# Performance work log

Hardware: AMD Instinct MI355X
Metric: run time of the kernel (lower is better)

The kernel has to match this reference:

```python
import jax, jax.numpy as jnp
import numpy as np

EPS = 1e-6


def _expand_mask(mask, D, H, W):
    # mask: (B,1,f,f,f) bool -> (B,1,D,H,W) via repeat_interleave on each spatial axis
    m = jnp.repeat(mask, D // mask.shape[2], axis=2)
    m = jnp.repeat(m, H // mask.shape[3], axis=3)
    m = jnp.repeat(m, W // mask.shape[4], axis=4)
    return m


def setup_inputs() -> dict:
    key = jax.random.key(0)
    ks = jax.random.split(key, 10)
    B, C, D, H, W = 2, 192, 32, 32, 32
    K, HID = 7, 4 * C
    x = jax.random.normal(ks[0], (B, C, D, H, W), dtype=jnp.float32)
    mask = jax.random.randint(ks[1], (B, 1, 8, 8, 8), 0, 2) > 0
    dw_w = jax.random.normal(ks[2], (C, 1, K, K, K), dtype=jnp.float32) * (1.0 / np.sqrt(K**3))
    dw_b = jnp.zeros((C,), dtype=jnp.float32)
    ln_w = jnp.ones((C,), dtype=jnp.float32)
    ln_b = jnp.zeros((C,), dtype=jnp.float32)
    w1 = jax.random.normal(ks[3], (C, HID), dtype=jnp.float32) * (1.0 / np.sqrt(C))
    b1 = jnp.zeros((HID,), dtype=jnp.float32)
    w2 = jax.random.normal(ks[4], (HID, C), dtype=jnp.float32) * (1.0 / np.sqrt(HID))
    b2 = jnp.zeros((C,), dtype=jnp.float32)
    gamma = jnp.full((C,), 1e-6, dtype=jnp.float32)
    return {"x": x, "mask": mask, "dw_w": dw_w, "dw_b": dw_b, "ln_w": ln_w,
            "ln_b": ln_b, "w1": w1, "b1": b1, "w2": w2, "b2": b2, "gamma": gamma}


def reference(x, mask, dw_w, dw_b, ln_w, ln_b, w1, b1, w2, b2, gamma):
    B, C, D, H, W = x.shape
    m = _expand_mask(mask, D, H, W)              # (B,1,D,H,W) bool
    mf = m.astype(x.dtype)

    # depthwise 3D conv, SAME padding (padding = kernel//2), groups = C
    y = jax.lax.conv_general_dilated(
        x, dw_w, window_strides=(1, 1, 1), padding='SAME',
        dimension_numbers=('NCDHW', 'OIDHW', 'NCDHW'),
        feature_group_count=C)
    y = y + dw_b[None, :, None, None, None]

    # channels_last: (B,D,H,W,C)
    y = jnp.transpose(y, (0, 2, 3, 4, 1))

    # sparse LayerNorm over channel dim: normalize all tokens, keep only active
    # (equivalent to gather->LN->scatter-into-zeros in the original)
    mu = jnp.mean(y, axis=-1, keepdims=True)
    var = jnp.mean(jnp.square(y - mu), axis=-1, keepdims=True)
    ln = (y - mu) * jax.lax.rsqrt(var + EPS) * ln_w + ln_b
    ln = ln * jnp.transpose(mf, (0, 2, 3, 4, 1))  # zero inactive tokens

    # pointwise MLP
    h = jax.nn.gelu(jnp.einsum('bdhwc,ce->bdhwe', ln, w1) + b1, approximate=False)
    o = jnp.einsum('bdhwe,ec->bdhwc', h, w2) + b2
    o = gamma * o

    # back to channels_first and final sparse mask
    o = jnp.transpose(o, (0, 4, 1, 2, 3)) * mf
    return o
```

## Files before the change

kernel.cpp:

```cpp
#include <hip/hip_runtime.h>
#include <hip/hip_bf16.h>

typedef __attribute__((ext_vector_type(2))) float f2v;
typedef __attribute__((ext_vector_type(4))) float f4v;
typedef __attribute__((ext_vector_type(8))) short bf8v;

#define NPOS 32768
#define CCH  192
#define HID  768

#define WS_Y    ((size_t)0)
#define WS_B1F  ((size_t)25165824)
#define WS_B2F  ((size_t)25460736)
#define WS_WPF  ((size_t)25755648)
#define WS_TOTAL ((size_t)26357760)

__device__ inline unsigned short f2bf(float f){
  unsigned int u = __float_as_uint(f);
  u += 0x7FFFu + ((u >> 16) & 1u);
  return (unsigned short)(u >> 16);
}
__device__ inline float bf2f(unsigned short s){
  return __uint_as_float(((unsigned int)s) << 16);
}
__device__ inline float gelu_f(float x){
  float u = 0.7978845608028654f * x * fmaf(0.044715f, x*x, 1.0f);
  float e = __expf(2.0f*u);
  float th = __fdividef(e - 1.0f, e + 1.0f);
  return 0.5f*x*(1.0f + th);
}

#define DOT2(A, X, W) \
  asm("v_dot2_f32_f16 %0, %1, %2, %0" : "+v"(A) : "v"(X), "s"(W))

__global__ __launch_bounds__(256, 6) void conv_dw_f16_kernel(
    const float* __restrict__ x, const float* __restrict__ dw_b,
    const unsigned int* __restrict__ wpf, unsigned short* __restrict__ yc)
{
  __shared__ unsigned short ring[22*528];

  int bid = blockIdx.x;
  int c = bid % 192;
  int r = bid / 192;
  int xq = r & 1, yq = (r >> 1) & 1, zh = (r >> 2) & 1, b = r >> 3;
  int tx0 = xq*16, ty0 = yq*16, zb = zh*16;

  int tid = threadIdx.x;
  const float* xsrc = x + ((size_t)(b*CCH + c))*NPOS;

  for (int idx = tid; idx < 2904; idx += 256) {
    int sl = idx / 132;
    int rem = idx - sl*132;
    int rr = rem / 6, ci = rem - rr*6;
    int zi = zb - 3 + sl, gy = ty0 - 3 + rr, gx = tx0 - 4 + 4*ci;
    f4v v = {0.f, 0.f, 0.f, 0.f};
    if ((unsigned)zi < 32u && (unsigned)gy < 32u && (unsigned)gx <= 28u)
      v = *(const f4v*)(xsrc + (size_t)zi*1024 + gy*32 + gx);
    union { _Float16 h[4]; uint2 u2; } pk;
    pk.h[0] = (_Float16)v[0]; pk.h[1] = (_Float16)v[1];
    pk.h[2] = (_Float16)v[2]; pk.h[3] = (_Float16)v[3];
    *(uint2*)(ring + sl*528 + rr*24 + ci*4) = pk.u2;
  }
  __syncthreads();

  int p = tid & 15, zl = tid >> 4;
  int px = p & 3, py = p >> 2;
  int y0 = py*4, px4 = px*4;
  const unsigned short* base = ring + zl*528 + y0*24 + px4;

  const unsigned int* wb = wpf + (size_t)c*392;

  float acc[4][4];
  #pragma unroll
  for (int i = 0; i < 4; ++i)
    #pragma unroll
    for (int j = 0; j < 4; ++j) acc[i][j] = 0.f;

  #pragma unroll 1
  for (int s = 0; s < 7; ++s) {
    const unsigned short* sb = base + s*528;
    const unsigned int* wrow = wb + s*56;
    #pragma unroll
    for (int rr = 0; rr < 10; ++rr) {
      const unsigned short* rb = sb + rr*24;
      uint2 q0 = *(const uint2*)(rb);
      uint2 q1 = *(const uint2*)(rb + 4);
      uint2 q2 = *(const uint2*)(rb + 8);
      unsigned int D[6] = {q0.x, q0.y, q1.x, q1.y, q2.x, q2.y};
      #pragma unroll
      for (int dy = 0; dy < 4; ++dy) {
        int ky = rr - dy;
        if (ky < 0 || ky > 6) continue;
        const unsigned int* wk = wrow + ky*8;
        #pragma unroll
        for (int t = 0; t < 4; ++t) {
          DOT2(acc[dy][0], D[t],   wk[t]);
          DOT2(acc[dy][1], D[t+1], wk[4+t]);
          DOT2(acc[dy][2], D[t+1], wk[t]);
          DOT2(acc[dy][3], D[t+2], wk[4+t]);
        }
      }
    }
  }

  float bias = dw_b[c];
  int z = zb + zl;
  int cz = z >> 2, cx = (tx0 >> 2) + px, cy = (ty0 >> 2) + py;
  int cell = cz*64 + cy*8 + cx;
  unsigned short* ybase = yc + (((size_t)(b*512 + cell))*192 + c)*64;
  int tokz = (z & 3)*16;
  #pragma unroll
  for (int dy = 0; dy < 4; ++dy) {
    ushort4 o;
    o.x = f2bf(acc[dy][0] + bias);
    o.y = f2bf(acc[dy][1] + bias);
    o.z = f2bf(acc[dy][2] + bias);
    o.w = f2bf(acc[dy][3] + bias);
    *(ushort4*)(ybase + tokz + dy*4) = o;
  }
}

__global__ __launch_bounds__(256) void conv_dw_f32_kernel(
    const float* __restrict__ x, const float* __restrict__ dw_w,
    const float* __restrict__ dw_b, unsigned short* __restrict__ yc)
{
  __shared__ float ring[22*528];

  int bid = blockIdx.x;
  int c = bid % 192;
  int r = bid / 192;
  int xq = r & 1, yq = (r >> 1) & 1, zh = (r >> 2) & 1, b = r >> 3;
  int tx0 = xq*16, ty0 = yq*16, zb = zh*16;

  int tid = threadIdx.x;
  const float* xsrc = x + ((size_t)(b*CCH + c))*NPOS;

  for (int idx = tid; idx < 2904; idx += 256) {
    int sl = idx / 132;
    int rem = idx - sl*132;
    int rr = rem / 6, ci = rem - rr*6;
    int zi = zb - 3 + sl, gy = ty0 - 3 + rr, gx = tx0 - 4 + 4*ci;
    f4v v = {0.f, 0.f, 0.f, 0.f};
    if ((unsigned)zi < 32u && (unsigned)gy < 32u && (unsigned)gx <= 28u)
      v = *(const f4v*)(xsrc + (size_t)zi*1024 + gy*32 + gx);
    *(f4v*)(ring + sl*528 + rr*24 + ci*4) = v;
  }
  __syncthreads();

  int p = tid & 15, zl = tid >> 4;
  int px = p & 3, py = p >> 2;
  int y0 = py*4, px4 = px*4;
  const float* base = ring + zl*528 + y0*24 + px4;
  const float* wbase = dw_w + (size_t)c*343;

  f2v acc[8];
  #pragma unroll
  for (int i = 0; i < 8; ++i) acc[i] = (f2v){0.f, 0.f};

  #pragma unroll 1
  for (int s = 0; s < 7; ++s) {
    const float* sb = base + s*528;
    f4v n0 = *(const f4v*)(sb);
    f4v n1 = *(const f4v*)(sb + 4);
    f4v n2 = *(const f4v*)(sb + 8);
    #pragma unroll
    for (int rr = 0; rr < 10; ++rr) {
      f4v r0 = n0, r1 = n1, r2 = n2;
      if (rr < 9) {
        n0 = *(const f4v*)(sb + (rr+1)*24);
        n1 = *(const f4v*)(sb + (rr+1)*24 + 4);
        n2 = *(const f4v*)(sb + (rr+1)*24 + 8);
      }
      f2v pr[10];
      pr[1] = (f2v){r0[1], r0[2]};
      pr[2] = (f2v){r0[2], r0[3]};
      pr[3] = (f2v){r0[3], r1[0]};
      pr[4] = (f2v){r1[0], r1[1]};
      pr[5] = (f2v){r1[1], r1[2]};
      pr[6] = (f2v){r1[2], r1[3]};
      pr[7] = (f2v){r1[3], r2[0]};
      pr[8] = (f2v){r2[0], r2[1]};
      pr[9] = (f2v){r2[1], r2[2]};
      #pragma unroll
      for (int dy = 0; dy < 4; ++dy) {
        int ky = rr - dy;
        if (ky < 0 || ky > 6) continue;
        #pragma unroll
        for (int kx = 0; kx < 7; ++kx) {
          float w = wbase[s*49 + ky*7 + kx];
          f2v wv = (f2v){w, w};
          acc[dy*2+0] = __builtin_elementwise_fma(wv, pr[kx+1], acc[dy*2+0]);
          acc[dy*2+1] = __builtin_elementwise_fma(wv, pr[kx+3], acc[dy*2+1]);
        }
      }
    }
  }

  float bias = dw_b[c];
  int z = zb + zl;
  int cz = z >> 2, cx = (tx0 >> 2) + px, cy = (ty0 >> 2) + py;
  int cell = cz*64 + cy*8 + cx;
  unsigned short* ybase = yc + (((size_t)(b*512 + cell))*192 + c)*64;
  int tokz = (z & 3)*16;
  #pragma unroll
  for (int dy = 0; dy < 4; ++dy) {
    ushort4 o;
    o.x = f2bf(acc[dy*2+0][0] + bias);
    o.y = f2bf(acc[dy*2+0][1] + bias);
    o.z = f2bf(acc[dy*2+1][0] + bias);
    o.w = f2bf(acc[dy*2+1][1] + bias);
    *(ushort4*)(ybase + tokz + dy*4) = o;
  }
}

__global__ __launch_bounds__(256) void prep_w_kernel(
    const float* __restrict__ w1, const float* __restrict__ w2,
    const float* __restrict__ dw_w,
    unsigned short* __restrict__ b1f, unsigned short* __restrict__ b2f,
    unsigned int* __restrict__ wpf)
{
  int gid = blockIdx.x*256 + threadIdx.x;
  if (gid < 18432) {
    int fi = gid;
    int lane = fi & 63, fr = fi >> 6;
    int nt = fr / 6, ks = fr - nt*6;
    int n  = nt*16 + (lane & 15);
    int kb = ks*32 + (lane >> 4)*8;
    #pragma unroll
    for (int j = 0; j < 8; ++j) b1f[fi*8 + j] = f2bf(w1[(kb+j)*HID + n]);
  } else if (gid < 36864) {
    int fi = gid - 18432;
    int lane = fi & 63, fr = fi >> 6;
    int nt = fr / 24, ks = fr - nt*24;
    int n  = nt*16 + (lane & 15);
    int kb = ks*32 + (lane >> 4)*8;
    #pragma unroll
    for (int j = 0; j < 8; ++j) b2f[fi*8 + j] = f2bf(w2[(kb+j)*CCH + n]);
  } else if (gid < 46272) {
    int ci = gid - 36864;
    int cch = ci / 49, t7 = ci - cch*49;
    const float* wr = dw_w + cch*343 + t7*7;
    float w[8];
    #pragma unroll
    for (int j = 0; j < 7; ++j) w[j] = wr[j];
    w[7] = 0.f;
    union { _Float16 h[2]; unsigned int u; } pk;
    #pragma unroll
    for (int t = 0; t < 4; ++t) {
      pk.h[0] = (t == 0) ? (_Float16)0.f : (_Float16)w[2*t-1];
      pk.h[1] = (_Float16)w[2*t];
      wpf[ci*8 + t] = pk.u;
    }
    #pragma unroll
    for (int t = 0; t < 4; ++t) {
      pk.h[0] = (_Float16)w[2*t];
      pk.h[1] = (_Float16)w[2*t+1];
      wpf[ci*8 + 4 + t] = pk.u;
    }
  }
}

__global__ __launch_bounds__(256) void mlp_kernel(
    const unsigned short* __restrict__ yc, const unsigned short* __restrict__ b1f,
    const unsigned short* __restrict__ b2f, const float* __restrict__ b1,
    const float* __restrict__ b2, const float* __restrict__ gamma,
    const float* __restrict__ ln_w, const float* __restrict__ ln_b,
    const int* __restrict__ mask, float* __restrict__ out)
{
  int bid = blockIdx.x;
  int b = bid >> 9, cell = bid & 511;
  int cz = cell >> 6, cy = (cell >> 3) & 7, cx = cell & 7;
  int z0 = cz*4, y0 = cy*4, x0 = cx*4;
  int tid = threadIdx.x, wave = tid >> 6, lane = tid & 63;
  int lq = lane >> 4, ln15 = lane & 15;

  if (mask[bid] == 0) {
    f4v z4 = {0.f, 0.f, 0.f, 0.f};
    #pragma unroll
    for (int pp = 0; pp < 12; ++pp) {
      int i4 = tid + 256*pp;
      int c = i4 >> 4, rem = i4 & 15;
      int dz = rem >> 2, dy = rem & 3;
      *(f4v*)(out + ((size_t)(b*CCH + c))*NPOS
                  + (size_t)(z0+dz)*1024 + (y0+dy)*32 + x0) = z4;
    }
    return;
  }

  __shared__ __align__(16) char uni[26112];
  unsigned short* ymat = (unsigned short*)uni;
  unsigned short* hbuf = (unsigned short*)uni;
  __shared__ unsigned short aFrag[12288];
  __shared__ float sred[2][4][64];
  __shared__ float murs[2][64];

  const unsigned short* ysrc = yc + (size_t)bid*12288;

  #pragma unroll
  for (int k = 0; k < 12; ++k) {
    int idx = tid + 256*k;
    int c = idx >> 4, t4 = idx & 15;
    *(ushort4*)(ymat + c*68 + t4*4) = *(const ushort4*)(ysrc + c*64 + t4*4);
  }
  __syncthreads();

  {
    int tok = tid & 63, part = tid >> 6;
    float S = 0.f, Q = 0.f;
    #pragma unroll
    for (int j = 0; j < 48; ++j) {
      float v = bf2f(ymat[(part*48 + j)*68 + tok]);
      S += v; Q = fmaf(v, v, Q);
    }
    sred[0][part][tok] = S; sred[1][part][tok] = Q;
  }
  __syncthreads();
  if (tid < 64) {
    float S = sred[0][0][tid] + sred[0][1][tid] + sred[0][2][tid] + sred[0][3][tid];
    float Q = sred[1][0][tid] + sred[1][1][tid] + sred[1][2][tid] + sred[1][3][tid];
    float m = S*(1.f/192.f);
    float var = Q*(1.f/192.f) - m*m;
    murs[0][tid] = m;
    murs[1][tid] = rsqrtf(var + 1e-6f);
  }
  __syncthreads();

  #pragma unroll
  for (int k = 0; k < 6; ++k) {
    int fi = tid + 256*k;
    int lane2 = fi & 63, rest = fi >> 6;
    int mt = rest / 6, ks = rest - mt*6;
    int tok = mt*16 + (lane2 & 15);
    int cc0 = ks*32 + (lane2 >> 4)*8;
    float m = murs[0][tok], rs = murs[1][tok];
    f4v lw0 = *(const f4v*)(ln_w + cc0), lw1 = *(const f4v*)(ln_w + cc0 + 4);
    f4v lb0 = *(const f4v*)(ln_b + cc0), lb1 = *(const f4v*)(ln_b + cc0 + 4);
    union { bf8v v; unsigned short u[8]; } pk;
    #pragma unroll
    for (int j = 0; j < 4; ++j) {
      float v0 = (bf2f(ymat[(cc0+j)*68 + tok])   - m)*rs*lw0[j] + lb0[j];
      float v1 = (bf2f(ymat[(cc0+4+j)*68 + tok]) - m)*rs*lw1[j] + lb1[j];
      pk.u[j] = f2bf(v0); pk.u[4+j] = f2bf(v1);
    }
    *(bf8v*)(aFrag + fi*8) = pk.v;
  }
  __syncthreads();

  f4v acc2[4][3];
  #pragma unroll
  for (int mt = 0; mt < 4; ++mt)
    #pragma unroll
    for (int nt = 0; nt < 3; ++nt)
      acc2[mt][nt] = (f4v){0.f, 0.f, 0.f, 0.f};

  const unsigned short* p1base = b1f + wave*2*3072 + lane*8;
  const unsigned short* p2base = b2f + wave*3*12288 + lane*8;

  bf8v B1r[12];
  #pragma unroll
  for (int i = 0; i < 12; ++i) {
    int jj = i / 6, ks = i - jj*6;
    B1r[i] = *(const bf8v*)(p1base + jj*3072 + ks*512);
  }

  #pragma unroll 1
  for (int ch = 0; ch < 6; ++ch) {
    bf8v B2r[12];
    const unsigned short* p2 = p2base + ch*2048;
    #pragma unroll
    for (int ks2 = 0; ks2 < 4; ++ks2)
      #pragma unroll
      for (int nt = 0; nt < 3; ++nt)
        B2r[ks2*3 + nt] = *(const bf8v*)(p2 + nt*12288 + ks2*512);

    f4v a1[2][4];
    #pragma unroll
    for (int jj = 0; jj < 2; ++jj)
      #pragma unroll
      for (int mt = 0; mt < 4; ++mt) a1[jj][mt] = (f4v){0.f,0.f,0.f,0.f};
    #pragma unroll
    for (int ks = 0; ks < 6; ++ks) {
      bf8v Af[4];
      #pragma unroll
      for (int mt = 0; mt < 4; ++mt)
        Af[mt] = *(const bf8v*)(aFrag + ((mt*6 + ks)*64 + lane)*8);
      #pragma unroll
      for (int jj = 0; jj < 2; ++jj)
        #pragma unroll
        for (int mt = 0; mt < 4; ++mt)
          a1[jj][mt] = __builtin_amdgcn_mfma_f32_16x16x32_bf16(Af[mt], B1r[jj*6+ks], a1[jj][mt], 0, 0, 0);
    }

    if (ch < 5) {
      const unsigned short* p1 = p1base + (ch+1)*24576;
      #pragma unroll
      for (int i = 0; i < 12; ++i) {
        int jj = i / 6, ks = i - jj*6;
        B1r[i] = *(const bf8v*)(p1 + jj*3072 + ks*512);
      }
    }

    #pragma unroll
    for (int jj = 0; jj < 2; ++jj) {
      float b1v = b1[(ch*8 + wave*2 + jj)*16 + ln15];
      int lane_hi = jj*2 + (ln15 >> 3);
      #pragma unroll
      for (int mt = 0; mt < 4; ++mt)
        #pragma unroll
        for (int rr = 0; rr < 4; ++rr) {
          float g = gelu_f(a1[jj][mt][rr] + b1v);
          int elem = ((mt*4 + wave)*64 + lane_hi*16 + (lq*4 + rr))*8 + (lane & 7);
          hbuf[elem] = f2bf(g);
        }
    }
    __syncthreads();
    #pragma unroll
    for (int ks2 = 0; ks2 < 4; ++ks2) {
      bf8v A2[4];
      #pragma unroll
      for (int mt = 0; mt < 4; ++mt)
        A2[mt] = *(const bf8v*)(hbuf + ((mt*4 + ks2)*64 + lane)*8);
      #pragma unroll
      for (int nt = 0; nt < 3; ++nt)
        #pragma unroll
        for (int mt = 0; mt < 4; ++mt)
          acc2[mt][nt] = __builtin_amdgcn_mfma_f32_16x16x32_bf16(A2[mt], B2r[ks2*3+nt], acc2[mt][nt], 0, 0, 0);
    }
    __syncthreads();
  }

  #pragma unroll
  for (int nt = 0; nt < 3; ++nt) {
    int c = (wave*3 + nt)*16 + ln15;
    float gm = gamma[c], bb = b2[c];
    size_t cbase = ((size_t)(b*CCH + c))*NPOS + (size_t)(y0 + lq)*32 + x0;
    #pragma unroll
    for (int mt = 0; mt < 4; ++mt) {
      f4v o;
      o[0] = gm*(acc2[mt][nt][0] + bb);
      o[1] = gm*(acc2[mt][nt][1] + bb);
      o[2] = gm*(acc2[mt][nt][2] + bb);
      o[3] = gm*(acc2[mt][nt][3] + bb);
      *(f4v*)(out + cbase + (size_t)(z0 + mt)*1024) = o;
    }
  }
}

extern "C" void kernel_launch(void* const* d_in, const int* in_sizes, int n_in,
                              void* d_out, int out_size, void* d_ws, size_t ws_size,
                              hipStream_t stream) {
  const float* x     = (const float*)d_in[0];
  const int*   mask  = (const int*)  d_in[1];
  const float* dw_w  = (const float*)d_in[2];
  const float* dw_b  = (const float*)d_in[3];
  const float* ln_w  = (const float*)d_in[4];
  const float* ln_b  = (const float*)d_in[5];
  const float* w1    = (const float*)d_in[6];
  const float* b1    = (const float*)d_in[7];
  const float* w2    = (const float*)d_in[8];
  const float* b2    = (const float*)d_in[9];
  const float* gamma = (const float*)d_in[10];
  float* out = (float*)d_out;
  char* ws = (char*)d_ws;

  unsigned short* yc  = (unsigned short*)(ws + WS_Y);
  unsigned short* b1f = (unsigned short*)(ws + WS_B1F);
  unsigned short* b2f = (unsigned short*)(ws + WS_B2F);
  unsigned int*   wpf = (unsigned int*)(ws + WS_WPF);

  bool wp_ok = ws_size >= WS_TOTAL;
  int prep_grid = wp_ok ? 181 : 144;
  prep_w_kernel<<<prep_grid, 256, 0, stream>>>(w1, w2, dw_w, b1f, b2f, wpf);
  if (wp_ok)
    conv_dw_f16_kernel<<<3072, 256, 0, stream>>>(x, dw_b, wpf, yc);
  else
    conv_dw_f32_kernel<<<3072, 256, 0, stream>>>(x, dw_w, dw_b, yc);
  mlp_kernel<<<1024, 256, 0, stream>>>(yc, b1f, b2f, b1, b2, gamma, ln_w, ln_b, mask, out);
}
```

Before: 270.3 us.

## Compute depthwise 3D conv with f16 MFMA using banded Toeplitz weight fragments

```diff
diff --git a/kernel.cpp b/kernel.cpp
--- a/kernel.cpp
+++ b/kernel.cpp
@@ -4,6 +4,7 @@
 typedef __attribute__((ext_vector_type(2))) float f2v;
 typedef __attribute__((ext_vector_type(4))) float f4v;
 typedef __attribute__((ext_vector_type(8))) short bf8v;
+typedef __attribute__((ext_vector_type(8))) _Float16 h8v;
 
 #define NPOS 32768
 #define CCH  192
@@ -13,7 +14,9 @@
 #define WS_B1F  ((size_t)25165824)
 #define WS_B2F  ((size_t)25460736)
 #define WS_WPF  ((size_t)25755648)
-#define WS_TOTAL ((size_t)26357760)
+#define WS_B3F  ((size_t)26056704)
+#define WS_TOTAL_MFMA ((size_t)35690496)
+#define WS_TOTAL_DOT2 ((size_t)26056704)
 
 __device__ inline unsigned short f2bf(float f){
   unsigned int u = __float_as_uint(f);
@@ -32,6 +35,94 @@
 
 #define DOT2(A, X, W) \
   asm("v_dot2_f32_f16 %0, %1, %2, %0" : "+v"(A) : "v"(X), "s"(W))
+
+#define ZSTR 712
+__global__ __launch_bounds__(256) void conv_mfma_kernel(
+    const float* __restrict__ x, const float* __restrict__ dw_b,
+    const unsigned short* __restrict__ b3f, unsigned short* __restrict__ yc)
+{
+  __shared__ unsigned short tile[22*ZSTR];
+
+  int bid = blockIdx.x;
+  int c = bid % 192;
+  int r = bid / 192;
+  int xq = r & 1, yq = (r >> 1) & 1, zh = (r >> 2) & 1, b = r >> 3;
+  int tx0 = xq*16, ty0 = yq*16, zb = zh*16;
+
+  int tid = threadIdx.x;
+  const float* xsrc = x + ((size_t)(b*CCH + c))*NPOS;
+
+  #pragma unroll
+  for (int it = 0; it < 8; ++it) {
+    int idx = tid + 256*it;
+    if (idx < 1936) {
+      int ci = idx & 3;
+      int row = idx >> 2;
+      int lz = row / 22, ly = row - lz*22;
+      int gz = zb - 3 + lz, gy = ty0 - 3 + ly;
+      f4v v0 = {0.f,0.f,0.f,0.f}, v1 = {0.f,0.f,0.f,0.f};
+      if (((unsigned)gz < 32u) & ((unsigned)gy < 32u) & (ci < 3)) {
+        int gx0 = tx0 - 4 + 8*ci;
+        const float* src = xsrc + (size_t)gz*1024 + gy*32;
+        if ((unsigned)gx0 <= 28u)     v0 = *(const f4v*)(src + gx0);
+        if ((unsigned)(gx0+4) <= 28u) v1 = *(const f4v*)(src + gx0 + 4);
+      }
+      h8v pk;
+      pk[0] = (_Float16)v0[0]; pk[1] = (_Float16)v0[1];
+      pk[2] = (_Float16)v0[2]; pk[3] = (_Float16)v0[3];
+      pk[4] = (_Float16)v1[0]; pk[5] = (_Float16)v1[1];
+      pk[6] = (_Float16)v1[2]; pk[7] = (_Float16)v1[3];
+      *(h8v*)(tile + lz*ZSTR + ly*32 + ci*8) = pk;
+    }
+  }
+  __syncthreads();
+
+  int wv = tid >> 6, lane = tid & 63;
+  int q = lane >> 4, zm = lane & 15;
+
+  const unsigned short* abase = tile + (size_t)zm*ZSTR + q*8;
+  const unsigned short* bbase = b3f + ((size_t)c*49)*512 + (size_t)lane*8;
+
+  f4v acc[4];
+  #pragma unroll
+  for (int t = 0; t < 4; ++t) acc[t] = (f4v){0.f,0.f,0.f,0.f};
+
+  h8v Bc = *(const h8v*)(bbase);
+  #pragma unroll 1
+  for (int kz = 0; kz < 7; ++kz) {
+    h8v Af[10];
+    #pragma unroll
+    for (int rr = 0; rr < 10; ++rr)
+      Af[rr] = *(const h8v*)(abase + kz*ZSTR + (4*wv + rr)*32);
+    #pragma unroll
+    for (int ky = 0; ky < 7; ++ky) {
+      int tap = kz*7 + ky;
+      int tnx = (tap < 48) ? tap + 1 : 48;
+      h8v Bn = *(const h8v*)(bbase + (size_t)tnx*512);
+      acc[0] = __builtin_amdgcn_mfma_f32_16x16x32_f16(Af[ky+0], Bc, acc[0], 0, 0, 0);
+      acc[1] = __builtin_amdgcn_mfma_f32_16x16x32_f16(Af[ky+1], Bc, acc[1], 0, 0, 0);
+      acc[2] = __builtin_amdgcn_mfma_f32_16x16x32_f16(Af[ky+2], Bc, acc[2], 0, 0, 0);
+      acc[3] = __builtin_amdgcn_mfma_f32_16x16x32_f16(Af[ky+3], Bc, acc[3], 0, 0, 0);
+      Bc = Bn;
+    }
+  }
+
+  float bias = dw_b[c];
+  int cz = zh*4 + q;
+  int cx = (tx0 >> 2) + (zm >> 2);
+  int xr = zm & 3;
+  int cy = (ty0 >> 2) + wv;
+  int cell = cz*64 + cy*8 + cx;
+  unsigned short* yb0 = yc + (((size_t)(b*512 + cell))*192 + c)*64 + xr;
+  #pragma unroll
+  for (int t = 0; t < 4; ++t) {
+    unsigned short* yb = yb0 + t*4;
+    yb[0]  = f2bf(acc[t][0] + bias);
+    yb[16] = f2bf(acc[t][1] + bias);
+    yb[32] = f2bf(acc[t][2] + bias);
+    yb[48] = f2bf(acc[t][3] + bias);
+  }
+}
 
 __global__ __launch_bounds__(256, 6) void conv_dw_f16_kernel(
     const float* __restrict__ x, const float* __restrict__ dw_b,
@@ -67,7 +158,6 @@
   int px = p & 3, py = p >> 2;
   int y0 = py*4, px4 = px*4;
   const unsigned short* base = ring + zl*528 + y0*24 + px4;
-
   const unsigned int* wb = wpf + (size_t)c*392;
 
   float acc[4][4];
@@ -217,7 +307,7 @@
     const float* __restrict__ w1, const float* __restrict__ w2,
     const float* __restrict__ dw_w,
     unsigned short* __restrict__ b1f, unsigned short* __restrict__ b2f,
-    unsigned int* __restrict__ wpf)
+    unsigned int* __restrict__ wpf, unsigned short* __restrict__ b3f)
 {
   int gid = blockIdx.x*256 + threadIdx.x;
   if (gid < 18432) {
@@ -257,6 +347,19 @@
       pk.h[1] = (_Float16)w[2*t+1];
       wpf[ci*8 + 4 + t] = pk.u;
     }
+  } else if (gid < 648384) {
+    int fi = gid - 46272;
+    int lane = fi & 63, frag = fi >> 6;
+    int cch = frag / 49, tap = frag - cch*49;
+    const float* wr = dw_w + cch*343 + tap*7;
+    int q = lane >> 4, n = lane & 15;
+    h8v pk;
+    #pragma unroll
+    for (int j = 0; j < 8; ++j) {
+      int t = q*8 + j - n - 1;
+      pk[j] = (t >= 0 && t <= 6) ? (_Float16)wr[t] : (_Float16)0.f;
+    }
+    *(h8v*)(b3f + (size_t)fi*8) = pk;
   }
 }
 
@@ -467,11 +570,15 @@
   unsigned short* b1f = (unsigned short*)(ws + WS_B1F);
   unsigned short* b2f = (unsigned short*)(ws + WS_B2F);
   unsigned int*   wpf = (unsigned int*)(ws + WS_WPF);
-
-  bool wp_ok = ws_size >= WS_TOTAL;
-  int prep_grid = wp_ok ? 181 : 144;
-  prep_w_kernel<<<prep_grid, 256, 0, stream>>>(w1, w2, dw_w, b1f, b2f, wpf);
-  if (wp_ok)
+  unsigned short* b3f = (unsigned short*)(ws + WS_B3F);
+
+  bool mfma_ok = ws_size >= WS_TOTAL_MFMA;
+  bool dot2_ok = ws_size >= WS_TOTAL_DOT2;
+  int prep_grid = mfma_ok ? 2533 : (dot2_ok ? 181 : 144);
+  prep_w_kernel<<<prep_grid, 256, 0, stream>>>(w1, w2, dw_w, b1f, b2f, wpf, b3f);
+  if (mfma_ok)
+    conv_mfma_kernel<<<3072, 256, 0, stream>>>(x, dw_b, b3f, yc);
+  else if (dot2_ok)
     conv_dw_f16_kernel<<<3072, 256, 0, stream>>>(x, dw_b, wpf, yc);
   else
     conv_dw_f32_kernel<<<3072, 256, 0, stream>>>(x, dw_w, dw_b, yc);
```

New measurement: 238.8 us. -11.6%, faster.
